# Kernel tuning notes

Hardware: AMD Instinct MI355X
Metric: run time of the kernel (lower is better)

## Reference

```python
import jax, jax.numpy as jnp
import numpy as np

H, W, C_IN, C_OUT, B = 256, 256, 64, 64, 2
NEG_SLOPE = 0.2


def make_grid_edges(h, w, b):
    """8-neighborhood grid edges + self-loops (GATConv add_self_loops), batched with node offsets."""
    idx = np.arange(h * w).reshape(h, w)
    src_l, dst_l = [], []
    for dr in (-1, 0, 1):
        for dc in (-1, 0, 1):
            rs = slice(max(0, -dr), h - max(0, dr))
            cs = slice(max(0, -dc), w - max(0, dc))
            dst = idx[rs, cs]
            src = idx[rs.start + dr:rs.stop + dr, cs.start + dc:cs.stop + dc]
            src_l.append(src.ravel())
            dst_l.append(dst.ravel())
    s = np.concatenate(src_l)
    d = np.concatenate(dst_l)
    offs = (np.arange(b) * h * w)[:, None]
    return (s[None] + offs).ravel().astype(np.int32), (d[None] + offs).ravel().astype(np.int32)


def setup_inputs() -> dict:
    key = jax.random.key(0)
    ks = jax.random.split(key, 7)
    x = jax.random.normal(ks[0], (B, C_IN, H, W), dtype=jnp.float32)
    pos_w = jax.random.normal(ks[1], (2, C_IN), dtype=jnp.float32) * (1.0 / np.sqrt(2.0))
    pos_b = jax.random.normal(ks[2], (C_IN,), dtype=jnp.float32) * 0.1
    lin_w = jax.random.normal(ks[3], (C_IN, C_OUT), dtype=jnp.float32) * (1.0 / np.sqrt(C_IN))
    att_src = jax.random.normal(ks[4], (C_OUT,), dtype=jnp.float32) * (1.0 / np.sqrt(C_OUT))
    att_dst = jax.random.normal(ks[5], (C_OUT,), dtype=jnp.float32) * (1.0 / np.sqrt(C_OUT))
    bias = jax.random.normal(ks[6], (C_OUT,), dtype=jnp.float32) * 0.1
    es, ed = make_grid_edges(H, W, B)
    return {"x": x, "pos_w": pos_w, "pos_b": pos_b, "lin_w": lin_w,
            "att_src": att_src, "att_dst": att_dst, "bias": bias,
            "edge_src": jnp.asarray(es), "edge_dst": jnp.asarray(ed)}


def reference(x, pos_w, pos_b, lin_w, att_src, att_dst, bias, edge_src, edge_dst):
    b, c, h, w = x.shape
    n = h * w
    num_nodes = b * n
    # positional encoding: pos[h,w] = (y, x) in [-1,1]
    px = jnp.linspace(-1.0, 1.0, w)
    py = jnp.linspace(-1.0, 1.0, h)
    gx, gy = jnp.meshgrid(px, py, indexing="xy")          # (H, W)
    pos = jnp.stack([gy, gx], axis=-1)                     # (H, W, 2)
    pe = pos @ pos_w + pos_b                               # (H, W, C)
    xg = (x + pe.transpose(2, 0, 1)[None]).transpose(0, 2, 3, 1).reshape(num_nodes, c)
    # GATConv, heads=1: linear transform, per-edge attention logits
    hfeat = xg @ lin_w                                     # (BN, Cout)
    a_src = hfeat @ att_src                                # (BN,)
    a_dst = hfeat @ att_dst                                # (BN,)
    e = jax.nn.leaky_relu(a_src[edge_src] + a_dst[edge_dst], NEG_SLOPE)  # (E,)
    # segment softmax over incoming edges of each target node
    m = jax.ops.segment_max(e, edge_dst, num_segments=num_nodes)
    p = jnp.exp(e - m[edge_dst])
    s = jax.ops.segment_sum(p, edge_dst, num_segments=num_nodes)
    alpha = p / s[edge_dst]                                # (E,)
    # scatter-add aggregation of weighted messages
    out = jax.ops.segment_sum(alpha[:, None] * hfeat[edge_src], edge_dst,
                              num_segments=num_nodes) + bias
    return out.reshape(b, h, w, -1).transpose(0, 3, 1, 2)
```

## Files before the change

kernel.cpp:

```cpp
#include <hip/hip_runtime.h>

#define HGT 256
#define WID 256
#define CH  64
#define NB  2
#define HW  (HGT * WID)
#define NODES (NB * HW)
#define NEG_SLOPE 0.2f

typedef float f32x16 __attribute__((ext_vector_type(16)));
typedef short short8 __attribute__((ext_vector_type(8)));

__device__ __forceinline__ unsigned short f2bf(float f) {
    union { float f; unsigned u; } v; v.f = f;
    unsigned r = v.u + 0x7FFF + ((v.u >> 16) & 1);
    return (unsigned short)(r >> 16);
}

__global__ __launch_bounds__(256) void gat_prep(
    const float* __restrict__ lin_w, const float* __restrict__ pos_w,
    const float* __restrict__ pos_b,
    float* __restrict__ W0, float* __restrict__ W1, float* __restrict__ Bc,
    unsigned short* __restrict__ wt)
{
    __shared__ float r0[4][64], r1[4][64], r2[4][64];
    const int tid = threadIdx.x;
    const int co  = tid & 63;
    const int ty  = tid >> 6;

    float w0 = 0.f, w1 = 0.f, bc = 0.f;
    #pragma unroll
    for (int p = 0; p < 16; ++p) {
        const int ci = ty * 16 + p;
        const float lwv = lin_w[ci * CH + co];
        w0 = fmaf(pos_w[ci],      lwv, w0);
        w1 = fmaf(pos_w[CH + ci], lwv, w1);
        bc = fmaf(pos_b[ci],      lwv, bc);
    }
    r0[ty][co] = w0; r1[ty][co] = w1; r2[ty][co] = bc;

    {
        const int pco = tid >> 2;
        const int cib = (tid & 3) * 16;
        unsigned u[8];
        #pragma unroll
        for (int e = 0; e < 16; e += 2) {
            const unsigned lo = f2bf(lin_w[(cib + e)     * CH + pco]);
            const unsigned hh = f2bf(lin_w[(cib + e + 1) * CH + pco]);
            u[e >> 1] = lo | (hh << 16);
        }
        uint4* dst = (uint4*)(wt + pco * CH + cib);
        dst[0] = make_uint4(u[0], u[1], u[2], u[3]);
        dst[1] = make_uint4(u[4], u[5], u[6], u[7]);
    }

    __syncthreads();
    if (ty == 0) {
        W0[co] = r0[0][co] + r0[1][co] + r0[2][co] + r0[3][co];
        W1[co] = r1[0][co] + r1[1][co] + r1[2][co] + r1[3][co];
        Bc[co] = r2[0][co] + r2[1][co] + r2[2][co] + r2[3][co];
    }
}

__global__ __launch_bounds__(256, 3) void gat_feat(
    const float* __restrict__ x, const float* __restrict__ att_src,
    const float* __restrict__ att_dst, const float* __restrict__ W0s,
    const float* __restrict__ W1s, const float* __restrict__ Bcs,
    const unsigned short* __restrict__ wt,
    unsigned short* __restrict__ hfeat, float* __restrict__ asrc,
    float* __restrict__ adst)
{
    const int tid  = threadIdx.x;
    const int lane = tid & 63;
    const int wid  = tid >> 6;
    const int hi   = lane >> 5;
    const int col  = lane & 31;

    const int g     = blockIdx.x * 4 + wid;
    const int node0 = g * 32;
    const int b     = node0 >> 16;
    const int hw    = (node0 & (HW - 1)) + col;
    const int node  = node0 + col;

    short8 a0[4], a1[4];
    #pragma unroll
    for (int ks = 0; ks < 4; ++ks) {
        a0[ks] = *(const short8*)(wt + col * CH        + ks * 16 + hi * 8);
        a1[ks] = *(const short8*)(wt + (32 + col) * CH + ks * 16 + hi * 8);
    }

    const float* xp = x + (size_t)b * CH * HW + hw;
    float xv[32];
    #pragma unroll
    for (int ks = 0; ks < 4; ++ks)
        #pragma unroll
        for (int e = 0; e < 8; ++e)
            xv[ks * 8 + e] = xp[(size_t)(16 * ks + 8 * hi + e) * HW];

    f32x16 acc0, acc1;
    #pragma unroll
    for (int k = 0; k < 16; ++k) { acc0[k] = 0.f; acc1[k] = 0.f; }

    #pragma unroll
    for (int ks = 0; ks < 4; ++ks) {
        short8 bk;
        #pragma unroll
        for (int e = 0; e < 8; ++e)
            bk[e] = (short)f2bf(xv[ks * 8 + e]);
        acc0 = __builtin_amdgcn_mfma_f32_32x32x16_bf16(a0[ks], bk, acc0, 0, 0, 0);
        acc1 = __builtin_amdgcn_mfma_f32_32x32x16_bf16(a1[ks], bk, acc1, 0, 0, 0);
    }

    const int ii = hw >> 8, jj = hw & 255;
    const float py = -1.f + (2.f / 255.f) * (float)ii;
    const float px = -1.f + (2.f / 255.f) * (float)jj;

    uint2* hq = (uint2*)hfeat + (size_t)b * 16 * HW + hw;
    float as = 0.f, ad = 0.f;

    #pragma unroll
    for (int t = 0; t < 2; ++t) {
        const f32x16 A = (t == 0) ? acc0 : acc1;
        #pragma unroll
        for (int q2 = 0; q2 < 4; ++q2) {
            const int cb = 32 * t + 8 * q2 + 4 * hi;
            const float4 w0 = *(const float4*)&W0s[cb];
            const float4 w1 = *(const float4*)&W1s[cb];
            const float4 bc = *(const float4*)&Bcs[cb];
            const float4 s4 = *(const float4*)&att_src[cb];
            const float4 d4 = *(const float4*)&att_dst[cb];
            const float h0 = A[4 * q2 + 0] + py * w0.x + px * w1.x + bc.x;
            const float h1 = A[4 * q2 + 1] + py * w0.y + px * w1.y + bc.y;
            const float h2 = A[4 * q2 + 2] + py * w0.z + px * w1.z + bc.z;
            const float h3 = A[4 * q2 + 3] + py * w0.w + px * w1.w + bc.w;
            as += h0 * s4.x + h1 * s4.y + h2 * s4.z + h3 * s4.w;
            ad += h0 * d4.x + h1 * d4.y + h2 * d4.z + h3 * d4.w;
            const unsigned u0 = (unsigned)f2bf(h0) | ((unsigned)f2bf(h1) << 16);
            const unsigned u1 = (unsigned)f2bf(h2) | ((unsigned)f2bf(h3) << 16);
            const int q = 8 * t + 2 * q2 + hi;
            hq[(size_t)q * HW] = make_uint2(u0, u1);
        }
    }

    as += __shfl_xor(as, 32);
    ad += __shfl_xor(ad, 32);
    if (hi == 0) { asrc[node] = as; adst[node] = ad; }
}

__global__ __launch_bounds__(256) void gat_aggr(
    const unsigned short* __restrict__ hfeat, const float* __restrict__ asrc,
    const float* __restrict__ adst, const float* __restrict__ bias,
    float* __restrict__ out)
{
    const int tid = threadIdx.x;
    const int tx  = tid & 63;
    const int ty  = tid >> 6;

    const int raw = blockIdx.x;
    const int wg  = (raw & 7) * 1024 + (raw >> 3);
    const int qg    = wg & 3;
    const int chunk = (wg >> 2) & 3;
    const int bi    = wg >> 4;
    const int i     = bi & (HGT - 1);
    const int b     = bi >> 8;
    const int j     = chunk * 64 + tx;
    const int hw    = i * WID + j;
    const int node  = b * HW + hw;
    const int q     = __builtin_amdgcn_readfirstlane(qg * 4 + ty);

    const float adv = adst[node];

    float w[9];
    int   off[9];
    float m = -1e30f;
    #pragma unroll
    for (int t = 0; t < 9; ++t) {
        const int dr = t / 3 - 1, dc = t % 3 - 1;
        const int r = i + dr, c = j + dc;
        const bool ok = (r >= 0) && (r < HGT) && (c >= 0) && (c < WID);
        off[t] = ok ? (dr * WID + dc) : 0;
        float ev = -1e30f;
        if (ok) {
            ev = asrc[node + off[t]] + adv;
            ev = (ev >= 0.f) ? ev : NEG_SLOPE * ev;
        }
        w[t] = ev;
        m = fmaxf(m, ev);
    }

    float s = 0.f;
    #pragma unroll
    for (int t = 0; t < 9; ++t) {
        const float p = (w[t] > -1e29f) ? __expf(w[t] - m) : 0.f;
        w[t] = p; s += p;
    }
    const float inv = 1.f / s;

    const uint2* hq = (const uint2*)hfeat + (size_t)(b * 16 + q) * HW + hw;

    float a0 = 0.f, a1 = 0.f, a2 = 0.f, a3 = 0.f;
    #pragma unroll
    for (int t = 0; t < 9; ++t) {
        const uint2 v  = hq[off[t]];
        const float wt = w[t] * inv;
        a0 = fmaf(wt, __uint_as_float(v.x << 16),         a0);
        a1 = fmaf(wt, __uint_as_float(v.x & 0xffff0000u), a1);
        a2 = fmaf(wt, __uint_as_float(v.y << 16),         a2);
        a3 = fmaf(wt, __uint_as_float(v.y & 0xffff0000u), a3);
    }

    float* ob = out + (size_t)(b * CH + q * 4) * HW + hw;
    ob[0 * (size_t)HW] = a0 + bias[q * 4 + 0];
    ob[1 * (size_t)HW] = a1 + bias[q * 4 + 1];
    ob[2 * (size_t)HW] = a2 + bias[q * 4 + 2];
    ob[3 * (size_t)HW] = a3 + bias[q * 4 + 3];
}

extern "C" void kernel_launch(void* const* d_in, const int* in_sizes, int n_in,
                              void* d_out, int out_size, void* d_ws, size_t ws_size,
                              hipStream_t stream) {
    const float* x       = (const float*)d_in[0];
    const float* pos_w   = (const float*)d_in[1];
    const float* pos_b   = (const float*)d_in[2];
    const float* lin_w   = (const float*)d_in[3];
    const float* att_src = (const float*)d_in[4];
    const float* att_dst = (const float*)d_in[5];
    const float* bias    = (const float*)d_in[6];

    float* out = (float*)d_out;
    char*  ws  = (char*)d_ws;
    unsigned short* hfeat = (unsigned short*)ws;
    float* asrc = (float*)(ws + (size_t)NODES * CH * 2);
    float* adst = asrc + NODES;
    float* W0   = adst + NODES;
    float* W1   = W0 + CH;
    float* Bc   = W1 + CH;
    unsigned short* wt = (unsigned short*)(Bc + CH);

    gat_prep<<<dim3(1), dim3(256), 0, stream>>>(lin_w, pos_w, pos_b, W0, W1, Bc, wt);
    gat_feat<<<dim3(1024), dim3(256), 0, stream>>>(
        x, att_src, att_dst, W0, W1, Bc, wt, hfeat, asrc, adst);
    gat_aggr<<<dim3(8192), dim3(256), 0, stream>>>(
        hfeat, asrc, adst, bias, out);
}
```

Baseline: 127.2 us.

## Fuse feature transform and neighbor aggregation into one tiled kernel via LDS

Merges the feature/attention-logit kernel and the aggregation kernel into a single kernel. Each block computes bf16 features and attention scalars for an 8x32 tile plus a one-pixel halo into shared memory, then does the 3x3 softmax aggregation from LDS. This removes the global round trip of the intermediate feature buffer and logits, and one launch. In exchange it recomputes the halo region (about 1.33x the matmul work), uses roughly 45KB of LDS per block, which limits occupancy, and launches only 512 blocks.

```diff
diff --git a/kernel.cpp b/kernel.cpp
--- a/kernel.cpp
+++ b/kernel.cpp
@@ -5,8 +5,14 @@
 #define CH  64
 #define NB  2
 #define HW  (HGT * WID)
-#define NODES (NB * HW)
 #define NEG_SLOPE 0.2f
+
+#define TR 8
+#define TC 32
+#define HR (TR + 2)
+#define HC (TC + 2)
+#define NN (HR * HC)
+#define NG ((NN + 31) / 32)
 
 typedef float f32x16 __attribute__((ext_vector_type(16)));
 typedef short short8 __attribute__((ext_vector_type(8)));
@@ -62,25 +68,28 @@
     }
 }
 
-__global__ __launch_bounds__(256, 3) void gat_feat(
+__global__ __launch_bounds__(256) void gat_fused(
     const float* __restrict__ x, const float* __restrict__ att_src,
-    const float* __restrict__ att_dst, const float* __restrict__ W0s,
-    const float* __restrict__ W1s, const float* __restrict__ Bcs,
-    const unsigned short* __restrict__ wt,
-    unsigned short* __restrict__ hfeat, float* __restrict__ asrc,
-    float* __restrict__ adst)
+    const float* __restrict__ att_dst, const float* __restrict__ W0g,
+    const float* __restrict__ W1g, const float* __restrict__ Bcg,
+    const unsigned short* __restrict__ wt, const float* __restrict__ bias,
+    float* __restrict__ outp)
 {
+    __shared__ uint2 hlds[16 * NN];
+    __shared__ float aslds[NN], adlds[NN];
+
     const int tid  = threadIdx.x;
     const int lane = tid & 63;
     const int wid  = tid >> 6;
     const int hi   = lane >> 5;
     const int col  = lane & 31;
 
-    const int g     = blockIdx.x * 4 + wid;
-    const int node0 = g * 32;
-    const int b     = node0 >> 16;
-    const int hw    = (node0 & (HW - 1)) + col;
-    const int node  = node0 + col;
+    const int blk  = blockIdx.x;
+    const int sblk = (blk & 7) * 64 + (blk >> 3);
+    const int b    = sblk >> 8;
+    const int tix  = sblk & 255;
+    const int i0   = (tix >> 3) * TR;
+    const int j0   = (tix & 7) * TC;
 
     short8 a0[4], a1[4];
     #pragma unroll
@@ -89,99 +98,91 @@
         a1[ks] = *(const short8*)(wt + (32 + col) * CH + ks * 16 + hi * 8);
     }
 
-    const float* xp = x + (size_t)b * CH * HW + hw;
-    float xv[32];
-    #pragma unroll
-    for (int ks = 0; ks < 4; ++ks)
-        #pragma unroll
-        for (int e = 0; e < 8; ++e)
-            xv[ks * 8 + e] = xp[(size_t)(16 * ks + 8 * hi + e) * HW];
-
-    f32x16 acc0, acc1;
-    #pragma unroll
-    for (int k = 0; k < 16; ++k) { acc0[k] = 0.f; acc1[k] = 0.f; }
-
-    #pragma unroll
-    for (int ks = 0; ks < 4; ++ks) {
-        short8 bk;
-        #pragma unroll
-        for (int e = 0; e < 8; ++e)
-            bk[e] = (short)f2bf(xv[ks * 8 + e]);
-        acc0 = __builtin_amdgcn_mfma_f32_32x32x16_bf16(a0[ks], bk, acc0, 0, 0, 0);
-        acc1 = __builtin_amdgcn_mfma_f32_32x32x16_bf16(a1[ks], bk, acc1, 0, 0, 0);
-    }
-
-    const int ii = hw >> 8, jj = hw & 255;
-    const float py = -1.f + (2.f / 255.f) * (float)ii;
-    const float px = -1.f + (2.f / 255.f) * (float)jj;
-
-    uint2* hq = (uint2*)hfeat + (size_t)b * 16 * HW + hw;
-    float as = 0.f, ad = 0.f;
-
-    #pragma unroll
-    for (int t = 0; t < 2; ++t) {
-        const f32x16 A = (t == 0) ? acc0 : acc1;
-        #pragma unroll
-        for (int q2 = 0; q2 < 4; ++q2) {
-            const int cb = 32 * t + 8 * q2 + 4 * hi;
-            const float4 w0 = *(const float4*)&W0s[cb];
-            const float4 w1 = *(const float4*)&W1s[cb];
-            const float4 bc = *(const float4*)&Bcs[cb];
-            const float4 s4 = *(const float4*)&att_src[cb];
-            const float4 d4 = *(const float4*)&att_dst[cb];
-            const float h0 = A[4 * q2 + 0] + py * w0.x + px * w1.x + bc.x;
-            const float h1 = A[4 * q2 + 1] + py * w0.y + px * w1.y + bc.y;
-            const float h2 = A[4 * q2 + 2] + py * w0.z + px * w1.z + bc.z;
-            const float h3 = A[4 * q2 + 3] + py * w0.w + px * w1.w + bc.w;
-            as += h0 * s4.x + h1 * s4.y + h2 * s4.z + h3 * s4.w;
-            ad += h0 * d4.x + h1 * d4.y + h2 * d4.z + h3 * d4.w;
-            const unsigned u0 = (unsigned)f2bf(h0) | ((unsigned)f2bf(h1) << 16);
-            const unsigned u1 = (unsigned)f2bf(h2) | ((unsigned)f2bf(h3) << 16);
-            const int q = 8 * t + 2 * q2 + hi;
-            hq[(size_t)q * HW] = make_uint2(u0, u1);
-        }
-    }
-
-    as += __shfl_xor(as, 32);
-    ad += __shfl_xor(ad, 32);
-    if (hi == 0) { asrc[node] = as; adst[node] = ad; }
-}
-
-__global__ __launch_bounds__(256) void gat_aggr(
-    const unsigned short* __restrict__ hfeat, const float* __restrict__ asrc,
-    const float* __restrict__ adst, const float* __restrict__ bias,
-    float* __restrict__ out)
-{
-    const int tid = threadIdx.x;
-    const int tx  = tid & 63;
-    const int ty  = tid >> 6;
-
-    const int raw = blockIdx.x;
-    const int wg  = (raw & 7) * 1024 + (raw >> 3);
-    const int qg    = wg & 3;
-    const int chunk = (wg >> 2) & 3;
-    const int bi    = wg >> 4;
-    const int i     = bi & (HGT - 1);
-    const int b     = bi >> 8;
-    const int j     = chunk * 64 + tx;
-    const int hw    = i * WID + j;
-    const int node  = b * HW + hw;
-    const int q     = __builtin_amdgcn_readfirstlane(qg * 4 + ty);
-
-    const float adv = adst[node];
+    for (int g = wid; g < NG; g += 4) {
+        int nd = g * 32 + col;
+        if (nd > NN - 1) nd = NN - 1;
+        const int r = nd / HC;
+        const int c = nd - r * HC;
+        int gi = i0 + r - 1; gi = gi < 0 ? 0 : (gi > HGT - 1 ? HGT - 1 : gi);
+        int gj = j0 + c - 1; gj = gj < 0 ? 0 : (gj > WID - 1 ? WID - 1 : gj);
+
+        const float* xp = x + (size_t)b * CH * HW + gi * WID + gj;
+        float xv[32];
+        #pragma unroll
+        for (int ks = 0; ks < 4; ++ks)
+            #pragma unroll
+            for (int e = 0; e < 8; ++e)
+                xv[ks * 8 + e] = xp[(size_t)(16 * ks + 8 * hi + e) * HW];
+
+        f32x16 acc0, acc1;
+        #pragma unroll
+        for (int k = 0; k < 16; ++k) { acc0[k] = 0.f; acc1[k] = 0.f; }
+
+        #pragma unroll
+        for (int ks = 0; ks < 4; ++ks) {
+            short8 bk;
+            #pragma unroll
+            for (int e = 0; e < 8; ++e)
+                bk[e] = (short)f2bf(xv[ks * 8 + e]);
+            acc0 = __builtin_amdgcn_mfma_f32_32x32x16_bf16(a0[ks], bk, acc0, 0, 0, 0);
+            acc1 = __builtin_amdgcn_mfma_f32_32x32x16_bf16(a1[ks], bk, acc1, 0, 0, 0);
+        }
+
+        const float py = -1.f + (2.f / 255.f) * (float)gi;
+        const float px = -1.f + (2.f / 255.f) * (float)gj;
+        float as = 0.f, ad = 0.f;
+
+        #pragma unroll
+        for (int t = 0; t < 2; ++t) {
+            const f32x16 A = (t == 0) ? acc0 : acc1;
+            #pragma unroll
+            for (int q2 = 0; q2 < 4; ++q2) {
+                const int cb = 32 * t + 8 * q2 + 4 * hi;
+                const float4 w0 = *(const float4*)&W0g[cb];
+                const float4 w1 = *(const float4*)&W1g[cb];
+                const float4 bc = *(const float4*)&Bcg[cb];
+                const float4 s4 = *(const float4*)&att_src[cb];
+                const float4 d4 = *(const float4*)&att_dst[cb];
+                const float h0 = A[4 * q2 + 0] + py * w0.x + px * w1.x + bc.x;
+                const float h1 = A[4 * q2 + 1] + py * w0.y + px * w1.y + bc.y;
+                const float h2 = A[4 * q2 + 2] + py * w0.z + px * w1.z + bc.z;
+                const float h3 = A[4 * q2 + 3] + py * w0.w + px * w1.w + bc.w;
+                as += h0 * s4.x + h1 * s4.y + h2 * s4.z + h3 * s4.w;
+                ad += h0 * d4.x + h1 * d4.y + h2 * d4.z + h3 * d4.w;
+                const unsigned u0 = (unsigned)f2bf(h0) | ((unsigned)f2bf(h1) << 16);
+                const unsigned u1 = (unsigned)f2bf(h2) | ((unsigned)f2bf(h3) << 16);
+                const int q = 8 * t + 2 * q2 + hi;
+                hlds[q * NN + nd] = make_uint2(u0, u1);
+            }
+        }
+
+        as += __shfl_xor(as, 32);
+        ad += __shfl_xor(ad, 32);
+        if (hi == 0) { aslds[nd] = as; adlds[nd] = ad; }
+    }
+
+    __syncthreads();
+
+    const int pr = tid >> 5;
+    const int pc = tid & 31;
+    const int i  = i0 + pr;
+    const int j  = j0 + pc;
+    const int nd = (pr + 1) * HC + (pc + 1);
+
+    const float adv = adlds[nd];
 
     float w[9];
-    int   off[9];
+    int   tp[9];
     float m = -1e30f;
     #pragma unroll
     for (int t = 0; t < 9; ++t) {
         const int dr = t / 3 - 1, dc = t % 3 - 1;
-        const int r = i + dr, c = j + dc;
-        const bool ok = (r >= 0) && (r < HGT) && (c >= 0) && (c < WID);
-        off[t] = ok ? (dr * WID + dc) : 0;
+        const int ri = i + dr, cj = j + dc;
+        const bool ok = (ri >= 0) && (ri < HGT) && (cj >= 0) && (cj < WID);
+        tp[t] = nd + dr * HC + dc;
         float ev = -1e30f;
         if (ok) {
-            ev = asrc[node + off[t]] + adv;
+            ev = aslds[tp[t]] + adv;
             ev = (ev >= 0.f) ? ev : NEG_SLOPE * ev;
         }
         w[t] = ev;
@@ -195,25 +196,27 @@
         w[t] = p; s += p;
     }
     const float inv = 1.f / s;
-
-    const uint2* hq = (const uint2*)hfeat + (size_t)(b * 16 + q) * HW + hw;
-
-    float a0 = 0.f, a1 = 0.f, a2 = 0.f, a3 = 0.f;
-    #pragma unroll
-    for (int t = 0; t < 9; ++t) {
-        const uint2 v  = hq[off[t]];
-        const float wt = w[t] * inv;
-        a0 = fmaf(wt, __uint_as_float(v.x << 16),         a0);
-        a1 = fmaf(wt, __uint_as_float(v.x & 0xffff0000u), a1);
-        a2 = fmaf(wt, __uint_as_float(v.y << 16),         a2);
-        a3 = fmaf(wt, __uint_as_float(v.y & 0xffff0000u), a3);
-    }
-
-    float* ob = out + (size_t)(b * CH + q * 4) * HW + hw;
-    ob[0 * (size_t)HW] = a0 + bias[q * 4 + 0];
-    ob[1 * (size_t)HW] = a1 + bias[q * 4 + 1];
-    ob[2 * (size_t)HW] = a2 + bias[q * 4 + 2];
-    ob[3 * (size_t)HW] = a3 + bias[q * 4 + 3];
+    #pragma unroll
+    for (int t = 0; t < 9; ++t) w[t] *= inv;
+
+    float* ob = outp + (size_t)b * CH * HW + i * WID + j;
+    #pragma unroll
+    for (int q = 0; q < 16; ++q) {
+        float a0v = 0.f, a1v = 0.f, a2v = 0.f, a3v = 0.f;
+        #pragma unroll
+        for (int t = 0; t < 9; ++t) {
+            const uint2 v  = hlds[q * NN + tp[t]];
+            const float wv = w[t];
+            a0v = fmaf(wv, __uint_as_float(v.x << 16),         a0v);
+            a1v = fmaf(wv, __uint_as_float(v.x & 0xffff0000u), a1v);
+            a2v = fmaf(wv, __uint_as_float(v.y << 16),         a2v);
+            a3v = fmaf(wv, __uint_as_float(v.y & 0xffff0000u), a3v);
+        }
+        ob[(size_t)(4 * q + 0) * HW] = a0v + bias[4 * q + 0];
+        ob[(size_t)(4 * q + 1) * HW] = a1v + bias[4 * q + 1];
+        ob[(size_t)(4 * q + 2) * HW] = a2v + bias[4 * q + 2];
+        ob[(size_t)(4 * q + 3) * HW] = a3v + bias[4 * q + 3];
+    }
 }
 
 extern "C" void kernel_launch(void* const* d_in, const int* in_sizes, int n_in,
@@ -227,19 +230,13 @@
     const float* att_dst = (const float*)d_in[5];
     const float* bias    = (const float*)d_in[6];
 
-    float* out = (float*)d_out;
-    char*  ws  = (char*)d_ws;
-    unsigned short* hfeat = (unsigned short*)ws;
-    float* asrc = (float*)(ws + (size_t)NODES * CH * 2);
-    float* adst = asrc + NODES;
-    float* W0   = adst + NODES;
+    float* outp = (float*)d_out;
+    float* W0   = (float*)d_ws;
     float* W1   = W0 + CH;
     float* Bc   = W1 + CH;
     unsigned short* wt = (unsigned short*)(Bc + CH);
 
     gat_prep<<<dim3(1), dim3(256), 0, stream>>>(lin_w, pos_w, pos_b, W0, W1, Bc, wt);
-    gat_feat<<<dim3(1024), dim3(256), 0, stream>>>(
-        x, att_src, att_dst, W0, W1, Bc, wt, hfeat, asrc, adst);
-    gat_aggr<<<dim3(8192), dim3(256), 0, stream>>>(
-        hfeat, asrc, adst, bias, out);
-}
+    gat_fused<<<dim3(512), dim3(256), 0, stream>>>(
+        x, att_src, att_dst, W0, W1, Bc, wt, bias, outp);
+}
```

Measured after the change: 139.3 us. 9.5% more time.
